# Optimization experiments

Measured on AMD Instinct MI355X. Metric: run time of the kernel, lower is better.

## Reference

```python
import jax, jax.numpy as jnp
import numpy as np

NUM_EXPERTS = 8

def setup_inputs() -> dict:
    key = jax.random.key(0)
    k1, k2, k3, k4, k5 = jax.random.split(key, 5)
    T, D, H, O, E, K = 4096, 1024, 2048, 1024, NUM_EXPERTS, 2
    hidden_states = jax.random.normal(k1, (T, D), dtype=jnp.float32)
    top_k_indices = jax.random.randint(k2, (T, K), 0, E, dtype=jnp.int64)
    top_k_weights = jax.random.uniform(k3, (T, K), dtype=jnp.float32)
    gate_up_proj = jax.random.normal(k4, (E, 2 * H, D), dtype=jnp.float32) * 0.02
    down_proj = jax.random.normal(k5, (E, O, H), dtype=jnp.float32) * 0.02
    return {
        "hidden_states": hidden_states,
        "top_k_indices": top_k_indices,
        "top_k_weights": top_k_weights,
        "gate_up_proj": gate_up_proj,
        "down_proj": down_proj,
    }


def _moe(hidden_states, top_k_weights, gate_up_proj, down_proj, top_k_indices):
    # Mathematically identical to the torch per-token-gather loop, expressed as
    # dense all-expert compute + sparse combine (non-selected experts get weight 0).
    T = hidden_states.shape[0]
    E = gate_up_proj.shape[0]
    # [T, E, 2H]
    gate_up = jnp.einsum('td,ehd->teh', hidden_states, gate_up_proj)
    gate, up = jnp.split(gate_up, 2, axis=-1)
    h = jax.nn.silu(gate) * up  # [T, E, H]
    expert_out = jnp.einsum('teh,eoh->teo', h, down_proj)  # [T, E, O]
    # combine weights: scatter top-k routing weights into [T, E]
    combine = jnp.zeros((T, E), dtype=hidden_states.dtype)
    rows = jnp.arange(T)[:, None]
    combine = combine.at[rows, top_k_indices].add(top_k_weights)
    return jnp.einsum('teo,te->to', expert_out, combine)


def reference(hidden_states, top_k_indices, top_k_weights, gate_up_proj, down_proj):
    return _moe(hidden_states, top_k_weights, gate_up_proj, down_proj, top_k_indices)
```

## Files before the change

kernel.cpp:

```cpp
#include <hip/hip_runtime.h>
#include <stdint.h>

#define TOKS 4096
#define DIM  1024
#define HID  2048
#define OUTD 1024
#define NE   8
#define MP   9216
#define NBR  72

typedef __bf16 bf16;
typedef bf16 bf16x8 __attribute__((ext_vector_type(8)));
typedef float f32x4 __attribute__((ext_vector_type(4)));
typedef __attribute__((address_space(1))) void gvoid;
typedef __attribute__((address_space(3))) void lvoid;

#define WGU_OFF  0ull
#define WD_OFF   (WGU_OFF + 67108864ull)
#define XG_OFF   (WD_OFF  + 33554432ull)
#define H_OFF    (XG_OFF  + 18874368ull)
#define TK_OFF   (H_OFF   + 37748736ull)
#define META_OFF (TK_OFF  + 36864ull)
#define T2S_OFF  (META_OFF + 1024ull)
#define O0_OFF   WGU_OFF
#define O1_OFF   (WGU_OFF + 18874368ull)

__device__ __forceinline__ unsigned short f2bf(float f) {
  union { float f; unsigned u; } v; v.f = f;
  unsigned r = (v.u + 0x7FFFu + ((v.u >> 16) & 1u)) >> 16;
  return (unsigned short)r;
}
__device__ __forceinline__ float bf2f(unsigned short h) {
  union { unsigned u; float f; } v; v.u = ((unsigned)h) << 16; return v.f;
}
__device__ __forceinline__ unsigned pack2(float a, float b) {
  return (unsigned)f2bf(a) | ((unsigned)f2bf(b) << 16);
}
__device__ __forceinline__ void cp16(const void* g, void* l) {
  __builtin_amdgcn_global_load_lds((gvoid*)(void*)g, (lvoid*)l, 16, 0, 0);
}

#define CONVB ((NE * 2 * HID * DIM + NE * OUTD * HID) / 4 / 1024)
__global__ __launch_bounds__(1024) void route_conv_kernel(
    const int* __restrict__ idx, int* __restrict__ table,
    int* __restrict__ slot_token, int* __restrict__ tok2slot,
    const float4* __restrict__ srcGu, uint2* __restrict__ dstGu,
    const float4* __restrict__ srcD, uint2* __restrict__ dstD) {
  if (blockIdx.x != 0) {
    const int n1 = NE * 2 * HID * DIM / 4;
    int i = (int)(blockIdx.x - 1) * 1024 + threadIdx.x;
    float4 v; uint2* dp;
    if (i < n1) { v = srcGu[i]; dp = dstGu + i; }
    else        { v = srcD[i - n1]; dp = dstD + (i - n1); }
    uint2 o; o.x = pack2(v.x, v.y); o.y = pack2(v.z, v.w);
    *dp = o;
    return;
  }
  __shared__ int cnt[NE], offs[NE], cur[NE];
  const int tid = threadIdx.x, lane = tid & 63;
  for (int i = tid; i < MP; i += 1024) slot_token[i] = -1;
  if (tid < NE) cnt[tid] = 0;
  __syncthreads();
  int myE[8];
#pragma unroll
  for (int c = 0; c < 8; ++c) myE[c] = idx[c * 1024 + tid];
#pragma unroll
  for (int c = 0; c < 8; ++c) {
    int e = myE[c];
#pragma unroll
    for (int ex = 0; ex < NE; ++ex) {
      unsigned long long m = __ballot(e == ex);
      if (lane == 0 && m) atomicAdd(&cnt[ex], __popcll(m));
    }
  }
  __syncthreads();
  if (tid == 0) {
    int cum = 0;
    for (int e = 0; e < NE; ++e) {
      offs[e] = cum; cur[e] = 0;
      int nb = (cnt[e] + 127) >> 7;
      int bb = cum >> 7;
      for (int b = 0; b < nb; ++b) table[bb + b] = e;
      cum += nb << 7;
    }
    for (int b = cum >> 7; b < NBR; ++b) table[b] = -1;
  }
  __syncthreads();
#pragma unroll
  for (int c = 0; c < 8; ++c) {
    int e = myE[c];
    int pos = 0;
#pragma unroll
    for (int ex = 0; ex < NE; ++ex) {
      unsigned long long m = __ballot(e == ex);
      if (e == ex) {
        int rank = __popcll(m & ((1ull << lane) - 1ull));
        int leader = __ffsll(m) - 1;
        int base = 0;
        if (lane == leader) base = atomicAdd(&cur[ex], __popcll(m));
        base = __shfl(base, leader);
        pos = offs[ex] + base + rank;
      }
    }
    slot_token[pos] = (c * 1024 + tid) >> 1;
    tok2slot[c * 1024 + tid] = pos;
  }
}

#define GATHER_B 4608
__global__ void gather_kernel(const float* __restrict__ X,
                              const int* __restrict__ slot_token,
                              uint4* __restrict__ Xg) {
  int gid = blockIdx.x * 256 + threadIdx.x;
  int row = gid >> 7, j = (gid & 127) << 3;
  int t = slot_token[row];
  uint4 o;
  if (t >= 0) {
    const float4* p = (const float4*)(X + (size_t)t * DIM + j);
    float4 a = p[0], b = p[1];
    o.x = pack2(a.x, a.y); o.y = pack2(a.z, a.w);
    o.z = pack2(b.x, b.y); o.w = pack2(b.z, b.w);
  } else {
    o = uint4{0u, 0u, 0u, 0u};
  }
  Xg[gid] = o;
}

__global__ void combine_kernel(const unsigned short* __restrict__ O0,
                               const unsigned short* __restrict__ O1,
                               const int* __restrict__ tok2slot,
                               const float* __restrict__ wts, float4* __restrict__ out) {
  int t = blockIdx.x, c = threadIdx.x;
  int s0 = tok2slot[2 * t], s1 = tok2slot[2 * t + 1];
  float w0 = wts[2 * t], w1 = wts[2 * t + 1];
  uint2 a0 = ((const uint2*)(O0 + (size_t)s0 * OUTD))[c];
  uint2 b0 = ((const uint2*)(O1 + (size_t)s0 * OUTD))[c];
  uint2 a1 = ((const uint2*)(O0 + (size_t)s1 * OUTD))[c];
  uint2 b1 = ((const uint2*)(O1 + (size_t)s1 * OUTD))[c];
  float4 o;
  o.x = w0 * (bf2f(a0.x & 0xFFFF) + bf2f(b0.x & 0xFFFF)) + w1 * (bf2f(a1.x & 0xFFFF) + bf2f(b1.x & 0xFFFF));
  o.y = w0 * (bf2f(a0.x >> 16)    + bf2f(b0.x >> 16))    + w1 * (bf2f(a1.x >> 16)    + bf2f(b1.x >> 16));
  o.z = w0 * (bf2f(a0.y & 0xFFFF) + bf2f(b0.y & 0xFFFF)) + w1 * (bf2f(a1.y & 0xFFFF) + bf2f(b1.y & 0xFFFF));
  o.w = w0 * (bf2f(a0.y >> 16)    + bf2f(b0.y >> 16))    + w1 * (bf2f(a1.y >> 16)    + bf2f(b1.y >> 16));
  out[(size_t)t * (OUTD / 4) + c] = o;
}

__global__ __launch_bounds__(256) void gemm1_kernel(
    const unsigned short* __restrict__ Xg,
    const unsigned short* __restrict__ Wgu,
    unsigned short* __restrict__ Hbuf,
    const int* __restrict__ table) {
  int e = table[blockIdx.y];
  if (e < 0) return;
  const int tid = threadIdx.x;
  const int lane = tid & 63, wave = tid >> 6;
  const int wm = wave >> 1, wn = wave & 1;
  const int lr = lane & 15, quad = lane >> 4;

  __shared__ bf16 As[128 * 64];
  __shared__ bf16 Bg[64 * 64];
  __shared__ bf16 Bu[64 * 64];

  const unsigned short* A_base  = Xg  + (size_t)blockIdx.y * 128 * DIM;
  const unsigned short* Wg_base = Wgu + (size_t)e * 2 * HID * DIM + (size_t)(blockIdx.x * 64) * DIM;
  const unsigned short* Wu_base = Wg_base + (size_t)HID * DIM;

  f32x4 accg[4][2] = {}; f32x4 accu[4][2] = {};

  for (int kt = 0; kt < DIM / 64; ++kt) {
    const int kb = kt * 64;
#pragma unroll
    for (int i = 0; i < 4; ++i) {
      int s = i * 256 + tid, row = s >> 3, pc = s & 7, gc = pc ^ (row & 7);
      cp16(A_base + (size_t)row * DIM + kb + gc * 8, (void*)(As + row * 64 + pc * 8));
    }
#pragma unroll
    for (int i = 0; i < 2; ++i) {
      int s = i * 256 + tid, row = s >> 3, pc = s & 7, gc = pc ^ (row & 7);
      cp16(Wg_base + (size_t)row * DIM + kb + gc * 8, (void*)(Bg + row * 64 + pc * 8));
      cp16(Wu_base + (size_t)row * DIM + kb + gc * 8, (void*)(Bu + row * 64 + pc * 8));
    }
    __syncthreads();
#pragma unroll
    for (int ks = 0; ks < 2; ++ks) {
      bf16x8 a[4], bg[2], bu[2];
#pragma unroll
      for (int i = 0; i < 4; ++i) {
        int row = wm * 64 + i * 16 + lr;
        int pc = (ks * 4 + quad) ^ (row & 7);
        a[i] = *(const bf16x8*)(As + row * 64 + pc * 8);
      }
#pragma unroll
      for (int j = 0; j < 2; ++j) {
        int row = wn * 32 + j * 16 + lr;
        int pc = (ks * 4 + quad) ^ (row & 7);
        bg[j] = *(const bf16x8*)(Bg + row * 64 + pc * 8);
        bu[j] = *(const bf16x8*)(Bu + row * 64 + pc * 8);
      }
#pragma unroll
      for (int i = 0; i < 4; ++i)
#pragma unroll
        for (int j = 0; j < 2; ++j) {
          accg[i][j] = __builtin_amdgcn_mfma_f32_16x16x32_bf16(a[i], bg[j], accg[i][j], 0, 0, 0);
          accu[i][j] = __builtin_amdgcn_mfma_f32_16x16x32_bf16(a[i], bu[j], accu[i][j], 0, 0, 0);
        }
    }
    __syncthreads();
  }

  const int rowBase = blockIdx.y * 128 + wm * 64;
  const int colBase = blockIdx.x * 64 + wn * 32;
#pragma unroll
  for (int i = 0; i < 4; ++i)
#pragma unroll
    for (int r = 0; r < 4; ++r) {
      int row = rowBase + i * 16 + quad * 4 + r;
#pragma unroll
      for (int j = 0; j < 2; ++j) {
        float g = accg[i][j][r], u = accu[i][j][r];
        float s = g / (1.0f + __expf(-g));
        Hbuf[(size_t)row * HID + colBase + j * 16 + lr] = f2bf(s * u);
      }
    }
}

__global__ __launch_bounds__(256) void gemm2_kernel(
    const unsigned short* __restrict__ Hbuf,
    const unsigned short* __restrict__ Wd,
    unsigned short* __restrict__ O0,
    unsigned short* __restrict__ O1,
    const int* __restrict__ table) {
  int e = table[blockIdx.y];
  if (e < 0) return;
  const int tid = threadIdx.x;
  const int lane = tid & 63, wave = tid >> 6;
  const int wm = wave >> 1, wn = wave & 1;
  const int lr = lane & 15, quad = lane >> 4;
  const int kslice = blockIdx.z;

  __shared__ bf16 As[128 * 64];
  __shared__ bf16 Bs[128 * 64];

  const unsigned short* A_base = Hbuf + (size_t)blockIdx.y * 128 * HID + kslice * (HID / 2);
  const unsigned short* B_base = Wd + (size_t)e * OUTD * HID + (size_t)(blockIdx.x * 128) * HID
                               + kslice * (HID / 2);

  f32x4 acc[4][4] = {};

  for (int kt = 0; kt < (HID / 2) / 64; ++kt) {
    const int kb = kt * 64;
#pragma unroll
    for (int i = 0; i < 4; ++i) {
      int s = i * 256 + tid, row = s >> 3, pc = s & 7, gc = pc ^ (row & 7);
      cp16(A_base + (size_t)row * HID + kb + gc * 8, (void*)(As + row * 64 + pc * 8));
      cp16(B_base + (size_t)row * HID + kb + gc * 8, (void*)(Bs + row * 64 + pc * 8));
    }
    __syncthreads();
#pragma unroll
    for (int ks = 0; ks < 2; ++ks) {
      bf16x8 a[4], b[4];
#pragma unroll
      for (int i = 0; i < 4; ++i) {
        int row = wm * 64 + i * 16 + lr;
        int pc = (ks * 4 + quad) ^ (row & 7);
        a[i] = *(const bf16x8*)(As + row * 64 + pc * 8);
      }
#pragma unroll
      for (int j = 0; j < 4; ++j) {
        int row = wn * 64 + j * 16 + lr;
        int pc = (ks * 4 + quad) ^ (row & 7);
        b[j] = *(const bf16x8*)(Bs + row * 64 + pc * 8);
      }
#pragma unroll
      for (int i = 0; i < 4; ++i)
#pragma unroll
        for (int j = 0; j < 4; ++j)
          acc[i][j] = __builtin_amdgcn_mfma_f32_16x16x32_bf16(a[i], b[j], acc[i][j], 0, 0, 0);
    }
    __syncthreads();
  }

  unsigned short* O = kslice ? O1 : O0;
  const int rowBase = blockIdx.y * 128 + wm * 64;
  const int colBase = blockIdx.x * 128 + wn * 64;
#pragma unroll
  for (int i = 0; i < 4; ++i)
#pragma unroll
    for (int r = 0; r < 4; ++r) {
      int row = rowBase + i * 16 + quad * 4 + r;
      unsigned short* Orow = O + (size_t)row * OUTD + colBase;
#pragma unroll
      for (int j = 0; j < 4; ++j)
        Orow[j * 16 + lr] = f2bf(acc[i][j][r]);
    }
}

extern "C" void kernel_launch(void* const* d_in, const int* in_sizes, int n_in,
                              void* d_out, int out_size, void* d_ws, size_t ws_size,
                              hipStream_t stream) {
  const float* X     = (const float*)d_in[0];
  const int*   idx   = (const int*)d_in[1];
  const float* wts   = (const float*)d_in[2];
  const float* WguF  = (const float*)d_in[3];
  const float* WdF   = (const float*)d_in[4];
  float* out = (float*)d_out;

  char* base = (char*)d_ws;
  unsigned short* Wgu = (unsigned short*)(base + WGU_OFF);
  unsigned short* Wd  = (unsigned short*)(base + WD_OFF);
  unsigned short* Xg  = (unsigned short*)(base + XG_OFF);
  unsigned short* Hb  = (unsigned short*)(base + H_OFF);
  unsigned short* O0  = (unsigned short*)(base + O0_OFF);
  unsigned short* O1  = (unsigned short*)(base + O1_OFF);
  int* slot_token = (int*)(base + TK_OFF);
  int* table      = (int*)(base + META_OFF);
  int* tok2slot   = (int*)(base + T2S_OFF);

  route_conv_kernel<<<1 + CONVB, 1024, 0, stream>>>(idx, table, slot_token, tok2slot,
      (const float4*)WguF, (uint2*)Wgu, (const float4*)WdF, (uint2*)Wd);
  gather_kernel<<<GATHER_B, 256, 0, stream>>>(X, slot_token, (uint4*)Xg);
  gemm1_kernel<<<dim3(HID / 64, NBR), 256, 0, stream>>>(Xg, Wgu, Hb, table);
  gemm2_kernel<<<dim3(OUTD / 128, NBR, 2), 256, 0, stream>>>(Hb, Wd, O0, O1, table);
  combine_kernel<<<TOKS, 256, 0, stream>>>(O0, O1, tok2slot, wts, (float4*)out);
}
```

Baseline: 411.4 us.

## Overlap down-projection weight conversion with gemm1 via extra blocks

Moves the fp32-to-bf16 conversion of the down-projection weights out of the routing/convert kernel and into extra blocks of the gemm1 launch (grid x widened from 32 to 40). Those extra 576 blocks grid-stride over the down weights while the GEMM blocks run. The aim is to hide the memory-bound conversion behind gemm1 compute instead of running it serially before the gather. The risk is that the converter blocks compete with GEMM blocks for bandwidth and CU slots, and the blockIdx.y ordering may delay GEMM tiles.

Result: no change. 406.3 us (-1.2%).

```diff
diff --git a/kernel.cpp b/kernel.cpp
--- a/kernel.cpp
+++ b/kernel.cpp
@@ -40,20 +40,16 @@
   __builtin_amdgcn_global_load_lds((gvoid*)(void*)g, (lvoid*)l, 16, 0, 0);
 }
 
-#define CONVB ((NE * 2 * HID * DIM + NE * OUTD * HID) / 4 / 1024)
+#define CONVB_GU (NE * 2 * HID * DIM / 4 / 1024)
 __global__ __launch_bounds__(1024) void route_conv_kernel(
     const int* __restrict__ idx, int* __restrict__ table,
     int* __restrict__ slot_token, int* __restrict__ tok2slot,
-    const float4* __restrict__ srcGu, uint2* __restrict__ dstGu,
-    const float4* __restrict__ srcD, uint2* __restrict__ dstD) {
+    const float4* __restrict__ srcGu, uint2* __restrict__ dstGu) {
   if (blockIdx.x != 0) {
-    const int n1 = NE * 2 * HID * DIM / 4;
     int i = (int)(blockIdx.x - 1) * 1024 + threadIdx.x;
-    float4 v; uint2* dp;
-    if (i < n1) { v = srcGu[i]; dp = dstGu + i; }
-    else        { v = srcD[i - n1]; dp = dstD + (i - n1); }
+    float4 v = srcGu[i];
     uint2 o; o.x = pack2(v.x, v.y); o.y = pack2(v.z, v.w);
-    *dp = o;
+    dstGu[i] = o;
     return;
   }
   __shared__ int cnt[NE], offs[NE], cur[NE];
@@ -145,11 +141,24 @@
   out[(size_t)t * (OUTD / 4) + c] = o;
 }
 
+#define WD_N4 (NE * OUTD * HID / 4)
+#define CVT_NB 576
 __global__ __launch_bounds__(256) void gemm1_kernel(
     const unsigned short* __restrict__ Xg,
     const unsigned short* __restrict__ Wgu,
     unsigned short* __restrict__ Hbuf,
-    const int* __restrict__ table) {
+    const int* __restrict__ table,
+    const float4* __restrict__ srcD, uint2* __restrict__ dstD) {
+  if (blockIdx.x >= 32) {
+    const int cid = (blockIdx.x - 32) + 8 * blockIdx.y;
+    const int NT = CVT_NB * 256;
+    for (int i = cid * 256 + (int)threadIdx.x; i < WD_N4; i += NT) {
+      float4 v = srcD[i];
+      uint2 o; o.x = pack2(v.x, v.y); o.y = pack2(v.z, v.w);
+      dstD[i] = o;
+    }
+    return;
+  }
   int e = table[blockIdx.y];
   if (e < 0) return;
   const int tid = threadIdx.x;
@@ -316,10 +325,11 @@
   int* table      = (int*)(base + META_OFF);
   int* tok2slot   = (int*)(base + T2S_OFF);
 
-  route_conv_kernel<<<1 + CONVB, 1024, 0, stream>>>(idx, table, slot_token, tok2slot,
-      (const float4*)WguF, (uint2*)Wgu, (const float4*)WdF, (uint2*)Wd);
+  route_conv_kernel<<<1 + CONVB_GU, 1024, 0, stream>>>(idx, table, slot_token, tok2slot,
+      (const float4*)WguF, (uint2*)Wgu);
   gather_kernel<<<GATHER_B, 256, 0, stream>>>(X, slot_token, (uint4*)Xg);
-  gemm1_kernel<<<dim3(HID / 64, NBR), 256, 0, stream>>>(Xg, Wgu, Hb, table);
+  gemm1_kernel<<<dim3(40, NBR), 256, 0, stream>>>(Xg, Wgu, Hb, table,
+      (const float4*)WdF, (uint2*)Wd);
   gemm2_kernel<<<dim3(OUTD / 128, NBR, 2), 256, 0, stream>>>(Hb, Wd, O0, O1, table);
   combine_kernel<<<TOKS, 256, 0, stream>>>(O0, O1, tok2slot, wts, (float4*)out);
 }
```
